# Optimization experiments

Measured on AMD Instinct MI355X. Metric: run time of the kernel, lower is better.

## Reference

```python
import jax, jax.numpy as jnp
import numpy as np

INF = 1e10  # stand-in for the original global INF constant
D_MODEL = 1024
N_HEADS = 16
SCALE = float(np.sqrt(D_MODEL))  # Attention is built with full d_key, so scale = sqrt(d_model)


def setup_inputs() -> dict:
    key = jax.random.key(0)
    ks = jax.random.split(key, 8)
    B, S, D = 4, 2048, D_MODEL
    s = 1.0 / np.sqrt(D)
    return {
        "query": jax.random.normal(ks[0], (B, S, D), jnp.float32),
        "key": jax.random.normal(ks[1], (B, S, D), jnp.float32),
        "value": jax.random.normal(ks[2], (B, S, D), jnp.float32),
        "wq": jax.random.normal(ks[3], (D, D), jnp.float32) * s,
        "bq": jnp.zeros((D,), jnp.float32),
        "wk": jax.random.normal(ks[4], (D, D), jnp.float32) * s,
        "bk": jnp.zeros((D,), jnp.float32),
        "wv": jax.random.normal(ks[5], (D, D), jnp.float32) * s,
        "bv": jnp.zeros((D,), jnp.float32),
        "wo": jax.random.normal(ks[6], (D, D), jnp.float32) * s,
        "bo": jnp.zeros((D,), jnp.float32),
    }


def reference(query, key, value, wq, bq, wk, bk, wv, bv, wo, bo):
    B, S, D = query.shape
    H = N_HEADS
    dh = D // H
    q = query @ wq + bq
    k = key @ wk + bk
    v = value @ wv + bv
    # split heads: [B, S, H, dh]
    q = q.reshape(B, S, H, dh)
    k = k.reshape(B, S, H, dh)
    v = v.reshape(B, S, H, dh)
    # raw dot products (unscaled), then causal mask subtracted (as in original),
    # then divide by sqrt(d_key) and softmax
    scores = jnp.einsum("bqhd,bkhd->bhqk", q, k)
    causal = jnp.triu(jnp.ones((S, S), scores.dtype), k=1) * INF
    scores = scores - causal  # broadcast over [B, H]
    attn = jax.nn.softmax(scores / SCALE, axis=-1)
    out = jnp.einsum("bhqk,bkhd->bqhd", attn, v).reshape(B, S, D)
    return out @ wo + bo
```

## Files before the change

kernel.cpp:

```cpp
#include <hip/hip_runtime.h>
#include <hip/hip_bf16.h>

typedef __bf16 bf16_t;
typedef __bf16 bf16x8 __attribute__((ext_vector_type(8)));
typedef float f32x4 __attribute__((ext_vector_type(4)));

#define MFMA16(a, b, c) __builtin_amdgcn_mfma_f32_16x16x32_bf16((a), (b), (c), 0, 0, 0)

static constexpr int S_LEN = 2048;
static constexpr int DM = 1024;
static constexpr int NH = 16;
static constexpr int DH = 64;

typedef const __attribute__((address_space(1))) unsigned int gu32;
typedef __attribute__((address_space(3))) unsigned int lu32;
__device__ __forceinline__ void gl_lds16(const void* src, void* dst) {
    __builtin_amdgcn_global_load_lds((gu32*)src, (lu32*)dst, 16, 0, 0);
}

struct WtArgs { const float* w[4]; bf16_t* o[4]; };

__global__ __launch_bounds__(256) void wt_kernel(WtArgs p) {
    int bid = blockIdx.x;
    int wi = bid >> 8;
    int tb = bid & 255;
    int k0 = (tb >> 4) * 64;
    int n0 = (tb & 15) * 64;
    const float* w = p.w[wi];
    bf16_t* o = p.o[wi];
    __shared__ bf16_t t[64 * 66];
    int tid = threadIdx.x;
#pragma unroll
    for (int i = 0; i < 4; ++i) {
        int f = tid + 256 * i;
        int row = f >> 4;
        int c4 = f & 15;
        f32x4 v = *reinterpret_cast<const f32x4*>(w + (size_t)(k0 + row) * DM + n0 + c4 * 4);
        int base = row * 66 + c4 * 4;
        t[base + 0] = (bf16_t)v[0];
        t[base + 1] = (bf16_t)v[1];
        t[base + 2] = (bf16_t)v[2];
        t[base + 3] = (bf16_t)v[3];
    }
    __syncthreads();
#pragma unroll
    for (int i = 0; i < 2; ++i) {
        int c = tid + 256 * i;
        int n = c >> 3;
        int ck = c & 7;
        union { bf16_t h[8]; uint4 u; } cv;
#pragma unroll
        for (int j = 0; j < 8; ++j) cv.h[j] = t[(ck * 8 + j) * 66 + n];
        *reinterpret_cast<uint4*>(o + (size_t)(n0 + n) * DM + k0 + ck * 8) = cv.u;
    }
}

template <int MODE>
__global__ __launch_bounds__(256) void gemm_k(const void* __restrict__ Ap,
                                              const bf16_t* __restrict__ BT,
                                              const float* __restrict__ bias,
                                              void* __restrict__ Cp, float alpha) {
    constexpr int K = 1024, N = 1024;
    constexpr int AS = (MODE == 1) ? 32 : 40;
    int bid = blockIdx.x;
    int bm = bid >> 3, bn = bid & 7;
    int tid = threadIdx.x;
    int w = tid >> 6, l = tid & 63;
    int g = l >> 4, lc = l & 15;

    __shared__ bf16_t a_buf[2][128 * AS];
    __shared__ bf16_t b_buf[2][128 * 32];

    f32x4 zero = {0.f, 0.f, 0.f, 0.f};
    f32x4 acc[4][4];
#pragma unroll
    for (int m = 0; m < 4; ++m)
#pragma unroll
        for (int n = 0; n < 4; ++n) acc[m][n] = zero;

    int m0 = bm * 128, n0 = bn * 128;
    const float* Af = (const float*)Ap;
    const bf16_t* Ab = (const bf16_t*)Ap;
    int wr = (w >> 1) * 64, wc = (w & 1) * 64;

    auto stage = [&](int buf, int kt) {
        int k0 = kt * 32;
        if constexpr (MODE != 1) {
#pragma unroll
            for (int i = 0; i < 4; ++i) {
                int f = tid + 256 * i;
                int row = f >> 3, c4 = f & 7;
                f32x4 v = *reinterpret_cast<const f32x4*>(Af + (size_t)(m0 + row) * K + k0 + c4 * 4);
                union { bf16_t h[4]; uint2 u; } cv;
                cv.h[0] = (bf16_t)v[0]; cv.h[1] = (bf16_t)v[1];
                cv.h[2] = (bf16_t)v[2]; cv.h[3] = (bf16_t)v[3];
                *reinterpret_cast<uint2*>(&a_buf[buf][row * 40 + c4 * 4]) = cv.u;
            }
        } else {
#pragma unroll
            for (int i = 0; i < 2; ++i) {
                int r16 = (w * 2 + i) * 16;
                int row = r16 + (l >> 2), ch = l & 3;
                gl_lds16(Ab + (size_t)(m0 + row) * K + k0 + ch * 8,
                         &a_buf[buf][r16 * 32]);
            }
        }
#pragma unroll
        for (int i = 0; i < 2; ++i) {
            int r16 = (w * 2 + i) * 16;
            int row = r16 + (l >> 2), ch = l & 3;
            gl_lds16(BT + (size_t)(n0 + row) * K + k0 + ch * 8,
                     &b_buf[buf][r16 * 32]);
        }
    };

    stage(0, 0);
    int cur = 0;
    for (int kt = 0; kt < K / 32; ++kt) {
        __syncthreads();
        if (kt + 1 < K / 32) stage(cur ^ 1, kt + 1);
        bf16x8 af[4], bfr[4];
#pragma unroll
        for (int m = 0; m < 4; ++m)
            af[m] = *reinterpret_cast<bf16x8*>(&a_buf[cur][(wr + m * 16 + lc) * AS + g * 8]);
#pragma unroll
        for (int n = 0; n < 4; ++n)
            bfr[n] = *reinterpret_cast<bf16x8*>(&b_buf[cur][(wc + n * 16 + lc) * 32 + g * 8]);
#pragma unroll
        for (int m = 0; m < 4; ++m)
#pragma unroll
            for (int n = 0; n < 4; ++n)
                acc[m][n] = MFMA16(af[m], bfr[n], acc[m][n]);
        cur ^= 1;
    }

    if constexpr (MODE == 2) {
#pragma unroll
        for (int n = 0; n < 4; ++n) {
            int ng = n0 + wc + n * 16 + lc;
            float bv = bias[ng];
            int h = ng >> 6, d = ng & 63;
#pragma unroll
            for (int m = 0; m < 4; ++m) {
                int s0g = m0 + wr + m * 16 + g * 4;
                int b = s0g >> 11, s0 = s0g & 2047;
                union { bf16_t hh[4]; uint2 u; } pk;
#pragma unroll
                for (int r = 0; r < 4; ++r)
                    pk.hh[r] = (bf16_t)((acc[m][n][r] + bv) * alpha);
                *reinterpret_cast<uint2*>(
                    &((bf16_t*)Cp)[(((size_t)(b * NH + h)) * DH + d) * S_LEN + s0]) = pk.u;
            }
        }
    } else {
#pragma unroll
        for (int n = 0; n < 4; ++n) {
            int ng = n0 + wc + n * 16 + lc;
            float bv = bias[ng];
#pragma unroll
            for (int m = 0; m < 4; ++m) {
#pragma unroll
                for (int r = 0; r < 4; ++r) {
                    int mg = m0 + wr + m * 16 + g * 4 + r;
                    float v = (acc[m][n][r] + bv) * alpha;
                    if constexpr (MODE == 0) {
                        int b = mg >> 11, s = mg & 2047, h = ng >> 6, d = ng & 63;
                        ((bf16_t*)Cp)[(((size_t)(b * NH + h)) * S_LEN + s) * DH + d] = (bf16_t)v;
                    } else {
                        ((float*)Cp)[(size_t)mg * N + ng] = v;
                    }
                }
            }
        }
    }
}

__global__ __launch_bounds__(256) void attn_kernel(const bf16_t* __restrict__ Qh,
                                                   const bf16_t* __restrict__ Kh,
                                                   const bf16_t* __restrict__ Vt,
                                                   bf16_t* __restrict__ AO) {
    int bid = blockIdx.x;
    int qt = 31 - (bid >> 6);
    int bh = bid & 63;
    int h = bh & 15;
    int b = bh >> 4;
    int tid = threadIdx.x;
    int w = tid >> 6, l = tid & 63;
    int g = l >> 4, lc = l & 15;
    int q0 = qt * 64 + w * 16;
    int q = q0 + lc;

    __shared__ bf16_t k_lds[2][64 * 64];
    __shared__ bf16_t v_lds[2][64 * 64];
    __shared__ bf16_t p_lds[4][16 * 64];

    size_t head_off = ((size_t)(b * NH + h)) * S_LEN * DH;
    const bf16_t* Kp = Kh + head_off;
    const bf16_t* Vp = Vt + head_off;

    bf16x8 qf[2];
    {
        const bf16_t* qp = Qh + head_off + (size_t)(q0 + lc) * DH + g * 8;
        qf[0] = *reinterpret_cast<const bf16x8*>(qp);
        qf[1] = *reinterpret_cast<const bf16x8*>(qp + 32);
    }

    f32x4 zero = {0.f, 0.f, 0.f, 0.f};
    f32x4 o_acc[4];
#pragma unroll
    for (int nt = 0; nt < 4; ++nt) o_acc[nt] = zero;
    float m_s = -1e30f, l_s = 0.f;

    int sw = lc & 7;

    auto stageKV = [&](int buf, int kv0) {
#pragma unroll
        for (int i = 0; i < 2; ++i) {
            int r8 = w * 16 + i * 8;
            int row = r8 + (l >> 3);
            int sc_ = (l & 7) ^ (row & 7);
            gl_lds16(Kp + (size_t)(kv0 + row) * DH + sc_ * 8, &k_lds[buf][r8 * 64]);
            gl_lds16(Vp + (size_t)row * S_LEN + kv0 + sc_ * 8, &v_lds[buf][r8 * 64]);
        }
    };

    stageKV(0, 0);
    int cur = 0;
    for (int t = 0; t <= qt; ++t) {
        int kv0 = t * 64;
        __syncthreads();
        if (t < qt) stageKV(cur ^ 1, kv0 + 64);

        f32x4 sc[4];
#pragma unroll
        for (int nt = 0; nt < 4; ++nt) {
            int row = nt * 16 + lc;
            bf16x8 kf0 = *reinterpret_cast<bf16x8*>(&k_lds[cur][row * 64 + ((g) ^ sw) * 8]);
            bf16x8 kf1 = *reinterpret_cast<bf16x8*>(&k_lds[cur][row * 64 + ((4 + g) ^ sw) * 8]);
            f32x4 s = zero;
            s = MFMA16(kf0, qf[0], s);
            s = MFMA16(kf1, qf[1], s);
            sc[nt] = s;
        }
        if (t == qt) {
#pragma unroll
            for (int nt = 0; nt < 4; ++nt)
#pragma unroll
                for (int r = 0; r < 4; ++r) {
                    int kv = kv0 + nt * 16 + g * 4 + r;
                    if (kv > q) sc[nt][r] = -1e30f;
                }
        }
        float tm = sc[0][0];
#pragma unroll
        for (int nt = 0; nt < 4; ++nt)
#pragma unroll
            for (int r = 0; r < 4; ++r) tm = fmaxf(tm, sc[nt][r]);
        tm = fmaxf(tm, __shfl_xor(tm, 16, 64));
        tm = fmaxf(tm, __shfl_xor(tm, 32, 64));
        float mn = fmaxf(m_s, tm);
        float al = __expf(m_s - mn);
        m_s = mn;
#pragma unroll
        for (int nt = 0; nt < 4; ++nt)
#pragma unroll
            for (int r = 0; r < 4; ++r) sc[nt][r] = __expf(sc[nt][r] - m_s);
        float ts = 0.f;
#pragma unroll
        for (int nt = 0; nt < 4; ++nt)
            ts += sc[nt][0] + sc[nt][1] + sc[nt][2] + sc[nt][3];
        ts += __shfl_xor(ts, 16, 64);
        ts += __shfl_xor(ts, 32, 64);
        l_s = l_s * al + ts;
#pragma unroll
        for (int r = 0; r < 4; ++r) {
            float alr = __shfl(al, g * 4 + r, 64);
#pragma unroll
            for (int nt = 0; nt < 4; ++nt) o_acc[nt][r] *= alr;
        }
#pragma unroll
        for (int nt = 0; nt < 4; ++nt) {
            union { bf16_t hh[4]; uint2 u; } pk;
#pragma unroll
            for (int r = 0; r < 4; ++r) pk.hh[r] = (bf16_t)sc[nt][r];
            int cu = nt * 2 + (g >> 1);
            *reinterpret_cast<uint2*>(
                &p_lds[w][lc * 64 + ((cu ^ sw) * 8) + (g & 1) * 4]) = pk.u;
        }
        bf16x8 pf0 = *reinterpret_cast<bf16x8*>(&p_lds[w][lc * 64 + ((g) ^ sw) * 8]);
        bf16x8 pf1 = *reinterpret_cast<bf16x8*>(&p_lds[w][lc * 64 + ((4 + g) ^ sw) * 8]);
#pragma unroll
        for (int nt = 0; nt < 4; ++nt) {
            int row = nt * 16 + lc;
            bf16x8 vf0 = *reinterpret_cast<bf16x8*>(&v_lds[cur][row * 64 + ((g) ^ sw) * 8]);
            bf16x8 vf1 = *reinterpret_cast<bf16x8*>(&v_lds[cur][row * 64 + ((4 + g) ^ sw) * 8]);
            o_acc[nt] = MFMA16(pf0, vf0, o_acc[nt]);
            o_acc[nt] = MFMA16(pf1, vf1, o_acc[nt]);
        }
        cur ^= 1;
    }

#pragma unroll
    for (int r = 0; r < 4; ++r) {
        float lr = __shfl(l_s, g * 4 + r, 64);
        float inv = 1.0f / lr;
        int qq = q0 + g * 4 + r;
        size_t base = ((size_t)b * S_LEN + qq) * DM + h * DH;
#pragma unroll
        for (int nt = 0; nt < 4; ++nt)
            AO[base + nt * 16 + lc] = (bf16_t)(o_acc[nt][r] * inv);
    }
}

extern "C" void kernel_launch(void* const* d_in, const int* in_sizes, int n_in,
                              void* d_out, int out_size, void* d_ws, size_t ws_size,
                              hipStream_t stream) {
    (void)in_sizes; (void)n_in; (void)out_size; (void)ws_size;
    const float* query = (const float*)d_in[0];
    const float* key   = (const float*)d_in[1];
    const float* value = (const float*)d_in[2];
    const float* wq = (const float*)d_in[3];
    const float* bq = (const float*)d_in[4];
    const float* wk = (const float*)d_in[5];
    const float* bk = (const float*)d_in[6];
    const float* wv = (const float*)d_in[7];
    const float* bv = (const float*)d_in[8];
    const float* wo = (const float*)d_in[9];
    const float* bo = (const float*)d_in[10];
    float* out = (float*)d_out;

    char* ws = (char*)d_ws;
    const size_t Mi = (size_t)1 << 20;
    bf16_t* wqT = (bf16_t*)(ws + 0 * Mi);
    bf16_t* wkT = (bf16_t*)(ws + 2 * Mi);
    bf16_t* wvT = (bf16_t*)(ws + 4 * Mi);
    bf16_t* woT = (bf16_t*)(ws + 6 * Mi);
    bf16_t* Qh  = (bf16_t*)(ws + 8 * Mi);
    bf16_t* Kh  = (bf16_t*)(ws + 24 * Mi);
    bf16_t* Vt  = (bf16_t*)(ws + 40 * Mi);
    bf16_t* AO  = (bf16_t*)(ws + 56 * Mi);

    WtArgs p;
    p.w[0] = wq; p.w[1] = wk; p.w[2] = wv; p.w[3] = wo;
    p.o[0] = wqT; p.o[1] = wkT; p.o[2] = wvT; p.o[3] = woT;
    wt_kernel<<<dim3(1024), dim3(256), 0, stream>>>(p);

    gemm_k<0><<<dim3(512), dim3(256), 0, stream>>>((const void*)query, wqT, bq, (void*)Qh, 0.03125f);
    gemm_k<0><<<dim3(512), dim3(256), 0, stream>>>((const void*)key,   wkT, bk, (void*)Kh, 1.0f);
    gemm_k<2><<<dim3(512), dim3(256), 0, stream>>>((const void*)value, wvT, bv, (void*)Vt, 1.0f);

    attn_kernel<<<dim3(2048), dim3(256), 0, stream>>>(Qh, Kh, Vt, AO);

    gemm_k<1><<<dim3(512), dim3(256), 0, stream>>>((const void*)AO, woT, bo, (void*)out, 1.0f);
}
```

Measured before the change: 242.5 us.

## Pre-cast activations to bf16, swizzle GEMM tiles, skip redundant softmax rescale

A separate cast kernel converts the fp32 query, key and value to bf16 into workspace regions that are later reused, so every projection GEMM can stage A with direct global-to-LDS loads instead of fp32 loads plus register conversion. GEMM block indexing is remapped so that consecutive blocks share a column tile of B, which should improve L2 reuse. In attention, the running-max rescale of l and the output accumulator is skipped when no lane's max increases. The cost is an extra kernel launch and an extra pass over the activations, plus a wave-wide vote and branch in the softmax loop.

```diff
diff --git a/kernel.cpp b/kernel.cpp
--- a/kernel.cpp
+++ b/kernel.cpp
@@ -55,20 +55,36 @@
     }
 }
 
+struct CastArgs { const float* s[3]; bf16_t* d[3]; };
+
+__global__ __launch_bounds__(256) void cast_kernel(CastArgs a) {
+    int bid = blockIdx.x;
+    int ti = bid >> 12;
+    size_t idx = (size_t)(((bid & 4095) << 8) | threadIdx.x) * 8;
+    const float* s = a.s[ti];
+    bf16_t* d = a.d[ti];
+    f32x4 v0 = *reinterpret_cast<const f32x4*>(s + idx);
+    f32x4 v1 = *reinterpret_cast<const f32x4*>(s + idx + 4);
+    union { bf16_t h[8]; uint4 u; } cv;
+#pragma unroll
+    for (int j = 0; j < 4; ++j) { cv.h[j] = (bf16_t)v0[j]; cv.h[4 + j] = (bf16_t)v1[j]; }
+    *reinterpret_cast<uint4*>(d + idx) = cv.u;
+}
+
 template <int MODE>
-__global__ __launch_bounds__(256) void gemm_k(const void* __restrict__ Ap,
+__global__ __launch_bounds__(256) void gemm_k(const bf16_t* __restrict__ Ab,
                                               const bf16_t* __restrict__ BT,
                                               const float* __restrict__ bias,
                                               void* __restrict__ Cp, float alpha) {
     constexpr int K = 1024, N = 1024;
-    constexpr int AS = (MODE == 1) ? 32 : 40;
     int bid = blockIdx.x;
-    int bm = bid >> 3, bn = bid & 7;
+    int bm = (bid & 7) * 8 + ((bid >> 3) & 7);
+    int bn = bid >> 6;
     int tid = threadIdx.x;
     int w = tid >> 6, l = tid & 63;
     int g = l >> 4, lc = l & 15;
 
-    __shared__ bf16_t a_buf[2][128 * AS];
+    __shared__ bf16_t a_buf[2][128 * 32];
     __shared__ bf16_t b_buf[2][128 * 32];
 
     f32x4 zero = {0.f, 0.f, 0.f, 0.f};
@@ -79,38 +95,16 @@
         for (int n = 0; n < 4; ++n) acc[m][n] = zero;
 
     int m0 = bm * 128, n0 = bn * 128;
-    const float* Af = (const float*)Ap;
-    const bf16_t* Ab = (const bf16_t*)Ap;
     int wr = (w >> 1) * 64, wc = (w & 1) * 64;
 
     auto stage = [&](int buf, int kt) {
         int k0 = kt * 32;
-        if constexpr (MODE != 1) {
-#pragma unroll
-            for (int i = 0; i < 4; ++i) {
-                int f = tid + 256 * i;
-                int row = f >> 3, c4 = f & 7;
-                f32x4 v = *reinterpret_cast<const f32x4*>(Af + (size_t)(m0 + row) * K + k0 + c4 * 4);
-                union { bf16_t h[4]; uint2 u; } cv;
-                cv.h[0] = (bf16_t)v[0]; cv.h[1] = (bf16_t)v[1];
-                cv.h[2] = (bf16_t)v[2]; cv.h[3] = (bf16_t)v[3];
-                *reinterpret_cast<uint2*>(&a_buf[buf][row * 40 + c4 * 4]) = cv.u;
-            }
-        } else {
-#pragma unroll
-            for (int i = 0; i < 2; ++i) {
-                int r16 = (w * 2 + i) * 16;
-                int row = r16 + (l >> 2), ch = l & 3;
-                gl_lds16(Ab + (size_t)(m0 + row) * K + k0 + ch * 8,
-                         &a_buf[buf][r16 * 32]);
-            }
-        }
 #pragma unroll
         for (int i = 0; i < 2; ++i) {
             int r16 = (w * 2 + i) * 16;
             int row = r16 + (l >> 2), ch = l & 3;
-            gl_lds16(BT + (size_t)(n0 + row) * K + k0 + ch * 8,
-                     &b_buf[buf][r16 * 32]);
+            gl_lds16(Ab + (size_t)(m0 + row) * K + k0 + ch * 8, &a_buf[buf][r16 * 32]);
+            gl_lds16(BT + (size_t)(n0 + row) * K + k0 + ch * 8, &b_buf[buf][r16 * 32]);
         }
     };
 
@@ -122,7 +116,7 @@
         bf16x8 af[4], bfr[4];
 #pragma unroll
         for (int m = 0; m < 4; ++m)
-            af[m] = *reinterpret_cast<bf16x8*>(&a_buf[cur][(wr + m * 16 + lc) * AS + g * 8]);
+            af[m] = *reinterpret_cast<bf16x8*>(&a_buf[cur][(wr + m * 16 + lc) * 32 + g * 8]);
 #pragma unroll
         for (int n = 0; n < 4; ++n)
             bfr[n] = *reinterpret_cast<bf16x8*>(&b_buf[cur][(wc + n * 16 + lc) * 32 + g * 8]);
@@ -258,9 +252,18 @@
             for (int r = 0; r < 4; ++r) tm = fmaxf(tm, sc[nt][r]);
         tm = fmaxf(tm, __shfl_xor(tm, 16, 64));
         tm = fmaxf(tm, __shfl_xor(tm, 32, 64));
-        float mn = fmaxf(m_s, tm);
-        float al = __expf(m_s - mn);
-        m_s = mn;
+        if (!__all(tm <= m_s)) {
+            float mn = fmaxf(m_s, tm);
+            float al = __expf(m_s - mn);
+            m_s = mn;
+            l_s *= al;
+#pragma unroll
+            for (int r = 0; r < 4; ++r) {
+                float alr = __shfl(al, g * 4 + r, 64);
+#pragma unroll
+                for (int nt = 0; nt < 4; ++nt) o_acc[nt][r] *= alr;
+            }
+        }
 #pragma unroll
         for (int nt = 0; nt < 4; ++nt)
 #pragma unroll
@@ -271,13 +274,7 @@
             ts += sc[nt][0] + sc[nt][1] + sc[nt][2] + sc[nt][3];
         ts += __shfl_xor(ts, 16, 64);
         ts += __shfl_xor(ts, 32, 64);
-        l_s = l_s * al + ts;
-#pragma unroll
-        for (int r = 0; r < 4; ++r) {
-            float alr = __shfl(al, g * 4 + r, 64);
-#pragma unroll
-            for (int nt = 0; nt < 4; ++nt) o_acc[nt][r] *= alr;
-        }
+        l_s += ts;
 #pragma unroll
         for (int nt = 0; nt < 4; ++nt) {
             union { bf16_t hh[4]; uint2 u; } pk;
@@ -339,17 +336,25 @@
     bf16_t* Kh  = (bf16_t*)(ws + 24 * Mi);
     bf16_t* Vt  = (bf16_t*)(ws + 40 * Mi);
     bf16_t* AO  = (bf16_t*)(ws + 56 * Mi);
+    bf16_t* Xq  = (bf16_t*)(ws + 24 * Mi);
+    bf16_t* Xk  = (bf16_t*)(ws + 40 * Mi);
+    bf16_t* Xv  = (bf16_t*)(ws + 56 * Mi);
 
     WtArgs p;
     p.w[0] = wq; p.w[1] = wk; p.w[2] = wv; p.w[3] = wo;
     p.o[0] = wqT; p.o[1] = wkT; p.o[2] = wvT; p.o[3] = woT;
     wt_kernel<<<dim3(1024), dim3(256), 0, stream>>>(p);
 
-    gemm_k<0><<<dim3(512), dim3(256), 0, stream>>>((const void*)query, wqT, bq, (void*)Qh, 0.03125f);
-    gemm_k<0><<<dim3(512), dim3(256), 0, stream>>>((const void*)key,   wkT, bk, (void*)Kh, 1.0f);
-    gemm_k<2><<<dim3(512), dim3(256), 0, stream>>>((const void*)value, wvT, bv, (void*)Vt, 1.0f);
+    CastArgs c;
+    c.s[0] = query; c.s[1] = key; c.s[2] = value;
+    c.d[0] = Xq; c.d[1] = Xk; c.d[2] = Xv;
+    cast_kernel<<<dim3(3 * 4096), dim3(256), 0, stream>>>(c);
+
+    gemm_k<0><<<dim3(512), dim3(256), 0, stream>>>(Xq, wqT, bq, (void*)Qh, 0.03125f);
+    gemm_k<0><<<dim3(512), dim3(256), 0, stream>>>(Xk, wkT, bk, (void*)Kh, 1.0f);
+    gemm_k<2><<<dim3(512), dim3(256), 0, stream>>>(Xv, wvT, bv, (void*)Vt, 1.0f);
 
     attn_kernel<<<dim3(2048), dim3(256), 0, stream>>>(Qh, Kh, Vt, AO);
 
-    gemm_k<1><<<dim3(512), dim3(256), 0, stream>>>((const void*)AO, woT, bo, (void*)out, 1.0f);
-}
+    gemm_k<1><<<dim3(512), dim3(256), 0, stream>>>(AO, woT, bo, (void*)out, 1.0f);
+}
```

After: 224.9 us. 1.08x faster.
